# Kernel tuning notes

Hardware: AMD Instinct MI355X
Metric: run time of the kernel (lower is better)

## Reference

```python
import jax, jax.numpy as jnp
import numpy as np

B, S, D = 8, 4096, 1280   # batch, tokens, model width (== down_dim == out_dim)
R = 64                    # lora rank (mid_dim)
EMBED_W = D + R * R + D   # [down | mid | up] slices of the per-sample embed


def setup_inputs() -> dict:
    key = jax.random.key(0)
    ks = jax.random.split(key, 6)
    x = jax.random.normal(ks[0], (B, S, D), dtype=jnp.float32)
    embed = jax.random.normal(ks[1], (B, EMBED_W), dtype=jnp.float32) * 0.05
    w_down = jax.random.normal(ks[2], (R, D), dtype=jnp.float32) * 0.02
    b_down = jnp.zeros((R,), dtype=jnp.float32)
    w_up = jax.random.normal(ks[3], (D, R), dtype=jnp.float32) * 0.02
    b_up = jnp.zeros((D,), dtype=jnp.float32)
    return {"x": x, "embed": embed, "w_down": w_down, "b_down": b_down,
            "w_up": w_up, "b_up": b_up}


def reference(x, embed, w_down, b_down, w_up, b_up):
    # down_forward: modulate input channels by per-sample down weight, then lora_down
    down_w = embed[:, :D]                          # [B, D]
    h = x * down_w[:, None, :]                     # [B, S, D]
    h = jnp.einsum('bsd,rd->bsr', h, w_down) + b_down   # lora_down Linear(D->R)
    # mid_forward: per-sample [R,R] weight, x_chunk @ W.T  (batched, no python loop)
    mid_w = embed[:, D:D + R * R].reshape(B, R, R)       # [B, R, R]
    h = jnp.einsum('bsr,bqr->bsq', h, mid_w)             # [B, S, R]
    # up_forward: lora_up then modulate output channels by per-sample up weight
    out = jnp.einsum('bsr,dr->bsd', h, w_up) + b_up      # lora_up Linear(R->D)
    up_w = embed[:, -D:]                                 # [B, D]
    out = out * up_w[:, None, :]
    return out
```

## Files before the change

kernel.cpp:

```cpp
#include <hip/hip_runtime.h>
#include <hip/hip_bf16.h>

#define NB 8
#define NS 4096
#define ND 1280
#define NR 64
#define EW 6656

typedef __attribute__((ext_vector_type(4))) float f4;
typedef __attribute__((ext_vector_type(8))) short bf8;

union BF8U { bf8 v; unsigned u[4]; };

__device__ __forceinline__ unsigned short f2bf(float f) {
  union { float f; unsigned u; } v; v.f = f;
  unsigned u = v.u + 0x7FFFu + ((v.u >> 16) & 1u);
  return (unsigned short)(u >> 16);
}

__device__ __forceinline__ unsigned pk2(float a, float b) {
  __hip_bfloat162 t = __float22bfloat162_rn(float2{a, b});
  return *reinterpret_cast<unsigned*>(&t);
}

__global__ __launch_bounds__(256) void prep_all(const float* __restrict__ embed,
                                                const float* __restrict__ w_down,
                                                const float* __restrict__ w_up,
                                                const float* __restrict__ b_down,
                                                unsigned short* __restrict__ W2F,
                                                unsigned short* __restrict__ W3FB,
                                                float* __restrict__ h2bias) {
  const int blk = blockIdx.x;
  const int t   = threadIdx.x;
  if (blk < 160) {
    const int b  = blk / 20;
    const int qg = (blk % 20) / 5;
    const int dg = blk % 5;
    __shared__ float mids[16][64];
    #pragma unroll
    for (int i = 0; i < 4; ++i) {
      int idx = t + i * 256;
      mids[idx >> 6][idx & 63] = embed[b * EW + ND + qg * 1024 + idx];
    }
    __syncthreads();
    const int d = dg * 256 + t;
    float acc[16];
    #pragma unroll
    for (int q = 0; q < 16; ++q) acc[q] = 0.f;
    for (int r = 0; r < 64; r += 8) {
      float wd[8];
      #pragma unroll
      for (int u = 0; u < 8; ++u) wd[u] = w_down[(r + u) * ND + d];
      #pragma unroll
      for (int u = 0; u < 8; ++u)
        #pragma unroll
        for (int q = 0; q < 16; ++q) acc[q] += mids[q][r + u] * wd[u];
    }
    const float dwn = embed[b * EW + d];
    const int kt = d >> 5, lanehi = (d & 31) >> 3, jj = d & 7;
    #pragma unroll
    for (int q = 0; q < 16; ++q)
      W2F[(((b * 40 + kt) * 4 + qg) << 9) + (lanehi * 16 + q) * 8 + jj] = f2bf(acc[q] * dwn);
  } else if (blk < 2720) {
    const int local = blk - 160;
    const int b  = local / 320;
    const int g  = (local % 320) * 256 + t;
    const int d  = g >> 6, q = g & 63;
    const int kt = q >> 5, nt = d >> 4;
    const int lanei = ((q & 31) >> 3) * 16 + (d & 15), jj = q & 7;
    const float upw = embed[b * EW + 5376 + d];
    W3FB[(size_t)b * 81920 + ((kt * 80 + nt) * 64 + lanei) * 8 + jj] = f2bf(w_up[g] * upw);
  } else {
    #pragma unroll
    for (int ii = 0; ii < 2; ++ii) {
      int id = ii * 256 + t;
      int bb = id >> 6, q = id & 63;
      float s = 0.f;
      for (int r = 0; r < 64; ++r) s += b_down[r] * embed[bb * EW + ND + q * 64 + r];
      h2bias[id] = s;
    }
  }
}

__global__ __launch_bounds__(256, 4) void k1_h2(const float* __restrict__ x,
                                                const unsigned short* __restrict__ W2F,
                                                const float* __restrict__ h2bias,
                                                uint4* __restrict__ h2F) {
  const int tid  = threadIdx.x;
  const int lane = tid & 63;
  const int w    = tid >> 6;
  const int kh   = w >> 1;
  const int rt   = w & 1;
  const int b    = blockIdx.x & 7;
  const int tile = blockIdx.x >> 3;
  const int lo16 = lane & 15;
  const int hi4  = lane >> 4;
  const int wrow = tile * 32 + rt * 16;

  __shared__ __align__(16) char smem[32768];
  float (*xs)[2][1024]    = (float (*)[2][1024])smem;
  float (*h2p)[2][16][68] = (float (*)[2][16][68])smem;

  const float* xbase = x + ((size_t)b * NS + wrow) * ND + kh * 640;
  const unsigned short* w2b = W2F + (size_t)b * 81920;

  #define ISSUE_DMA(ck, buf)                                                         \
    _Pragma("unroll")                                                                \
    for (int it = 0; it < 4; ++it) {                                                 \
      const int rloc = it * 4 + hi4;                                                 \
      const int cf   = lo16 ^ rloc;                                                  \
      const float* src = xbase + (size_t)rloc * ND + (ck) * 64 + cf * 4;             \
      __builtin_amdgcn_global_load_lds((__attribute__((address_space(1))) void*)src, \
          (__attribute__((address_space(3))) void*)&xs[w][buf][it * 256], 16, 0, 0); \
    }

  f4 acc[4] = {};
  bf8 bw[8];

  ISSUE_DMA(0, 0)
  {
    const unsigned short* wp = w2b + (((kh * 10) * 8) << 9) + lane * 8;
    #pragma unroll
    for (int i = 0; i < 8; ++i) bw[i] = *(const bf8*)(wp + (i << 9));
  }

  for (int ck = 0; ck < 10; ++ck) {
    const int buf = ck & 1;
    bf8 bn[8];
    if (ck < 9) {
      ISSUE_DMA(ck + 1, buf ^ 1)
      const unsigned short* wp = w2b + (size_t)(((kh * 10 + ck + 1) * 8) << 9) + lane * 8;
      #pragma unroll
      for (int i = 0; i < 8; ++i) bn[i] = *(const bf8*)(wp + (i << 9));
      asm volatile("s_waitcnt vmcnt(12)" ::: "memory");
    } else {
      asm volatile("s_waitcnt vmcnt(0)" ::: "memory");
    }
    const f4* xp = (const f4*)&xs[w][buf][0];
    f4 a0 = xp[lo16 * 16 + ((hi4 * 2)     ^ lo16)];
    f4 a1 = xp[lo16 * 16 + ((hi4 * 2 + 1) ^ lo16)];
    f4 a2 = xp[lo16 * 16 + ((hi4 * 2 + 8) ^ lo16)];
    f4 a3 = xp[lo16 * 16 + ((hi4 * 2 + 9) ^ lo16)];
    BF8U af0, af1;
    af0.u[0] = pk2(a0[0], a0[1]); af0.u[1] = pk2(a0[2], a0[3]);
    af0.u[2] = pk2(a1[0], a1[1]); af0.u[3] = pk2(a1[2], a1[3]);
    af1.u[0] = pk2(a2[0], a2[1]); af1.u[1] = pk2(a2[2], a2[3]);
    af1.u[2] = pk2(a3[0], a3[1]); af1.u[3] = pk2(a3[2], a3[3]);
    #pragma unroll
    for (int nt = 0; nt < 4; ++nt)
      acc[nt] = __builtin_amdgcn_mfma_f32_16x16x32_bf16(af0.v, bw[nt], acc[nt], 0, 0, 0);
    #pragma unroll
    for (int nt = 0; nt < 4; ++nt)
      acc[nt] = __builtin_amdgcn_mfma_f32_16x16x32_bf16(af1.v, bw[4 + nt], acc[nt], 0, 0, 0);
    if (ck < 9) {
      #pragma unroll
      for (int i = 0; i < 8; ++i) bw[i] = bn[i];
    }
  }

  __syncthreads();

  #pragma unroll
  for (int nt = 0; nt < 4; ++nt)
    #pragma unroll
    for (int j = 0; j < 4; ++j)
      h2p[kh][rt][hi4 * 4 + j][nt * 16 + lo16] = acc[nt][j];
  __syncthreads();

  const int q0 = kh * 32 + hi4 * 8;
  f4 u0 = *(const f4*)&h2p[0][rt][lo16][q0];
  f4 u1 = *(const f4*)&h2p[0][rt][lo16][q0 + 4];
  f4 v0 = *(const f4*)&h2p[1][rt][lo16][q0];
  f4 v1 = *(const f4*)&h2p[1][rt][lo16][q0 + 4];
  f4 c0 = *(const f4*)(h2bias + b * 64 + q0);
  f4 c1 = *(const f4*)(h2bias + b * 64 + q0 + 4);
  float s[8];
  #pragma unroll
  for (int j = 0; j < 4; ++j) {
    s[j]     = u0[j] + v0[j] + c0[j];
    s[4 + j] = u1[j] + v1[j] + c1[j];
  }
  uint4 pk;
  pk.x = pk2(s[0], s[1]); pk.y = pk2(s[2], s[3]);
  pk.z = pk2(s[4], s[5]); pk.w = pk2(s[6], s[7]);
  h2F[(size_t)(((b * 256 + tile * 2 + rt) * 2 + kh) * 64 + lane)] = pk;
}

__global__ __launch_bounds__(256, 4) void k2_out(const uint4* __restrict__ h2F,
                                                 const float* __restrict__ embed,
                                                 const float* __restrict__ b_up,
                                                 const unsigned short* __restrict__ W3FB,
                                                 float* __restrict__ out) {
  const int tid  = threadIdx.x;
  const int lane = tid & 63;
  const int w    = tid >> 6;
  const int kh   = w >> 1;
  const int rt   = w & 1;
  const int b    = blockIdx.x & 7;
  const int t2   = blockIdx.x >> 3;
  const int lo16 = lane & 15;
  const int hi4  = lane >> 4;

  __shared__ __align__(16) float lds[4][16][36];
  __shared__ __align__(16) float pbs[1280];

  const int tile16 = t2 * 2 + rt;
  uint4 hv0 = h2F[(size_t)(((b * 256 + tile16) * 2 + 0) * 64 + lane)];
  uint4 hv1 = h2F[(size_t)(((b * 256 + tile16) * 2 + 1) * 64 + lane)];

  const float* upw = embed + b * EW + 5376;
  #pragma unroll
  for (int i = 0; i < 5; ++i) {
    const int idx = i * 256 + tid;
    pbs[idx] = b_up[idx] * upw[idx];
  }
  __syncthreads();

  BF8U ha0, ha1;
  ha0.u[0] = hv0.x; ha0.u[1] = hv0.y; ha0.u[2] = hv0.z; ha0.u[3] = hv0.w;
  ha1.u[0] = hv1.x; ha1.u[1] = hv1.y; ha1.u[2] = hv1.z; ha1.u[3] = hv1.w;

  const unsigned short* w3b = W3FB + (size_t)b * 81920;
  float* outp = out + ((size_t)b * NS + t2 * 32 + rt * 16) * ND + kh * 640;
  const int dtbase = kh * 40;

  bf8 wb00 = *(const bf8*)(w3b + (size_t)((dtbase)      * 64 + lane) * 8);
  bf8 wb01 = *(const bf8*)(w3b + (size_t)((80 + dtbase) * 64 + lane) * 8);
  bf8 wb10 = *(const bf8*)(w3b + (size_t)((dtbase + 1)      * 64 + lane) * 8);
  bf8 wb11 = *(const bf8*)(w3b + (size_t)((80 + dtbase + 1) * 64 + lane) * 8);

  for (int c = 0; c < 20; ++c) {
    f4 o0 = {}, o1 = {};
    o0 = __builtin_amdgcn_mfma_f32_16x16x32_bf16(wb00, ha0.v, o0, 0, 0, 0);
    o0 = __builtin_amdgcn_mfma_f32_16x16x32_bf16(wb01, ha1.v, o0, 0, 0, 0);
    o1 = __builtin_amdgcn_mfma_f32_16x16x32_bf16(wb10, ha0.v, o1, 0, 0, 0);
    o1 = __builtin_amdgcn_mfma_f32_16x16x32_bf16(wb11, ha1.v, o1, 0, 0, 0);
    if (c < 19) {
      const int dt = dtbase + (c + 1) * 2;
      wb00 = *(const bf8*)(w3b + (size_t)(dt * 64 + lane) * 8);
      wb01 = *(const bf8*)(w3b + (size_t)((80 + dt) * 64 + lane) * 8);
      wb10 = *(const bf8*)(w3b + (size_t)((dt + 1) * 64 + lane) * 8);
      wb11 = *(const bf8*)(w3b + (size_t)((80 + dt + 1) * 64 + lane) * 8);
    }
    #pragma unroll
    for (int i = 0; i < 2; ++i) {
      const f4 oi = i ? o1 : o0;
      const int dl = kh * 640 + c * 32 + i * 16 + hi4 * 4;
      f4 pbv = *(const f4*)&pbs[dl];
      f4 r;
      #pragma unroll
      for (int j = 0; j < 4; ++j) r[j] = oi[j] + pbv[j];
      *(f4*)&lds[w][lo16][i * 16 + hi4 * 4] = r;
    }
    #pragma unroll
    for (int k = 0; k < 2; ++k) {
      const int rr = k * 8 + (lane >> 3);
      f4 v = *(const f4*)&lds[w][rr][(lane & 7) * 4];
      *(f4*)(outp + (size_t)rr * ND + c * 32 + (lane & 7) * 4) = v;
    }
  }
}

extern "C" void kernel_launch(void* const* d_in, const int* in_sizes, int n_in,
                              void* d_out, int out_size, void* d_ws, size_t ws_size,
                              hipStream_t stream) {
  const float* x      = (const float*)d_in[0];
  const float* embed  = (const float*)d_in[1];
  const float* w_down = (const float*)d_in[2];
  const float* b_down = (const float*)d_in[3];
  const float* w_up   = (const float*)d_in[4];
  const float* b_up   = (const float*)d_in[5];
  float* out = (float*)d_out;

  char* ws = (char*)d_ws;
  unsigned short* W2F  = (unsigned short*)ws;
  unsigned short* W3FB = (unsigned short*)(ws + 1310720);
  float* h2bias        = (float*)(ws + 2621440);
  uint4* h2F           = (uint4*)(ws + 2623488);

  prep_all<<<2721, 256, 0, stream>>>(embed, w_down, w_up, b_down, W2F, W3FB, h2bias);
  k1_h2   <<<1024, 256, 0, stream>>>(x, W2F, h2bias, h2F);
  k2_out  <<<1024, 256, 0, stream>>>(h2F, embed, b_up, W3FB, out);
}
```

Before: 102.9 us.

## Fuse down-projection and up-projection kernels into one mega kernel via LDS

Merges the k1_h2 and k2_out kernels into a single kernel. The bf16 rank-64 intermediate now passes through shared memory instead of a global buffer, which removes one launch and the global write and read of h2. The per-sample up bias and h2 bias are staged in LDS at kernel start. The W3 prefetch in the output loop is also moved ahead of the MFMAs into separate registers. In exchange, register and LDS pressure per block rise and the two phases lose independent scheduling.

```diff
diff --git a/kernel.cpp b/kernel.cpp
--- a/kernel.cpp
+++ b/kernel.cpp
@@ -82,10 +82,13 @@
   }
 }
 
-__global__ __launch_bounds__(256, 4) void k1_h2(const float* __restrict__ x,
-                                                const unsigned short* __restrict__ W2F,
-                                                const float* __restrict__ h2bias,
-                                                uint4* __restrict__ h2F) {
+__global__ __launch_bounds__(256, 4) void mega(const float* __restrict__ x,
+                                               const float* __restrict__ embed,
+                                               const float* __restrict__ b_up,
+                                               const unsigned short* __restrict__ W2F,
+                                               const unsigned short* __restrict__ W3FB,
+                                               const float* __restrict__ h2bias,
+                                               float* __restrict__ out) {
   const int tid  = threadIdx.x;
   const int lane = tid & 63;
   const int w    = tid >> 6;
@@ -97,9 +100,23 @@
   const int hi4  = lane >> 4;
   const int wrow = tile * 32 + rt * 16;
 
-  __shared__ __align__(16) char smem[32768];
-  float (*xs)[2][1024]    = (float (*)[2][1024])smem;
-  float (*h2p)[2][16][68] = (float (*)[2][16][68])smem;
+  __shared__ __align__(16) char pool[32768];
+  __shared__ __align__(16) float pbs[1280];
+  __shared__ float hb[64];
+  float (*xs)[2][1024]    = (float (*)[2][1024])pool;
+  float (*h2p)[2][16][68] = (float (*)[2][16][68])pool;
+  float (*ldsT)[16][36]   = (float (*)[16][36])pool;
+  uint4* pkx              = (uint4*)(pool + 28672);
+
+  if (tid < 64) hb[tid] = h2bias[b * 64 + tid];
+  {
+    const float* upw = embed + b * EW + 5376;
+    #pragma unroll
+    for (int i = 0; i < 5; ++i) {
+      const int idx = i * 256 + tid;
+      pbs[idx] = b_up[idx] * upw[idx];
+    }
+  }
 
   const float* xbase = x + ((size_t)b * NS + wrow) * ND + kh * 640;
   const unsigned short* w2b = W2F + (size_t)b * 81920;
@@ -167,81 +184,56 @@
       h2p[kh][rt][hi4 * 4 + j][nt * 16 + lo16] = acc[nt][j];
   __syncthreads();
 
-  const int q0 = kh * 32 + hi4 * 8;
-  f4 u0 = *(const f4*)&h2p[0][rt][lo16][q0];
-  f4 u1 = *(const f4*)&h2p[0][rt][lo16][q0 + 4];
-  f4 v0 = *(const f4*)&h2p[1][rt][lo16][q0];
-  f4 v1 = *(const f4*)&h2p[1][rt][lo16][q0 + 4];
-  f4 c0 = *(const f4*)(h2bias + b * 64 + q0);
-  f4 c1 = *(const f4*)(h2bias + b * 64 + q0 + 4);
-  float s[8];
-  #pragma unroll
-  for (int j = 0; j < 4; ++j) {
-    s[j]     = u0[j] + v0[j] + c0[j];
-    s[4 + j] = u1[j] + v1[j] + c1[j];
-  }
-  uint4 pk;
-  pk.x = pk2(s[0], s[1]); pk.y = pk2(s[2], s[3]);
-  pk.z = pk2(s[4], s[5]); pk.w = pk2(s[6], s[7]);
-  h2F[(size_t)(((b * 256 + tile * 2 + rt) * 2 + kh) * 64 + lane)] = pk;
-}
-
-__global__ __launch_bounds__(256, 4) void k2_out(const uint4* __restrict__ h2F,
-                                                 const float* __restrict__ embed,
-                                                 const float* __restrict__ b_up,
-                                                 const unsigned short* __restrict__ W3FB,
-                                                 float* __restrict__ out) {
-  const int tid  = threadIdx.x;
-  const int lane = tid & 63;
-  const int w    = tid >> 6;
-  const int kh   = w >> 1;
-  const int rt   = w & 1;
-  const int b    = blockIdx.x & 7;
-  const int t2   = blockIdx.x >> 3;
-  const int lo16 = lane & 15;
-  const int hi4  = lane >> 4;
-
-  __shared__ __align__(16) float lds[4][16][36];
-  __shared__ __align__(16) float pbs[1280];
-
-  const int tile16 = t2 * 2 + rt;
-  uint4 hv0 = h2F[(size_t)(((b * 256 + tile16) * 2 + 0) * 64 + lane)];
-  uint4 hv1 = h2F[(size_t)(((b * 256 + tile16) * 2 + 1) * 64 + lane)];
-
-  const float* upw = embed + b * EW + 5376;
-  #pragma unroll
-  for (int i = 0; i < 5; ++i) {
-    const int idx = i * 256 + tid;
-    pbs[idx] = b_up[idx] * upw[idx];
+  {
+    const int q0 = kh * 32 + hi4 * 8;
+    f4 u0 = *(const f4*)&h2p[0][rt][lo16][q0];
+    f4 u1 = *(const f4*)&h2p[0][rt][lo16][q0 + 4];
+    f4 v0 = *(const f4*)&h2p[1][rt][lo16][q0];
+    f4 v1 = *(const f4*)&h2p[1][rt][lo16][q0 + 4];
+    float s[8];
+    #pragma unroll
+    for (int j = 0; j < 4; ++j) {
+      s[j]     = u0[j] + v0[j] + hb[q0 + j];
+      s[4 + j] = u1[j] + v1[j] + hb[q0 + 4 + j];
+    }
+    uint4 pk;
+    pk.x = pk2(s[0], s[1]); pk.y = pk2(s[2], s[3]);
+    pk.z = pk2(s[4], s[5]); pk.w = pk2(s[6], s[7]);
+    pkx[(rt * 2 + kh) * 64 + lane] = pk;
   }
   __syncthreads();
 
   BF8U ha0, ha1;
-  ha0.u[0] = hv0.x; ha0.u[1] = hv0.y; ha0.u[2] = hv0.z; ha0.u[3] = hv0.w;
-  ha1.u[0] = hv1.x; ha1.u[1] = hv1.y; ha1.u[2] = hv1.z; ha1.u[3] = hv1.w;
+  {
+    uint4 hv0 = pkx[(rt * 2 + 0) * 64 + lane];
+    uint4 hv1 = pkx[(rt * 2 + 1) * 64 + lane];
+    ha0.u[0] = hv0.x; ha0.u[1] = hv0.y; ha0.u[2] = hv0.z; ha0.u[3] = hv0.w;
+    ha1.u[0] = hv1.x; ha1.u[1] = hv1.y; ha1.u[2] = hv1.z; ha1.u[3] = hv1.w;
+  }
 
   const unsigned short* w3b = W3FB + (size_t)b * 81920;
-  float* outp = out + ((size_t)b * NS + t2 * 32 + rt * 16) * ND + kh * 640;
+  float* outp = out + ((size_t)b * NS + tile * 32 + rt * 16) * ND + kh * 640;
   const int dtbase = kh * 40;
 
-  bf8 wb00 = *(const bf8*)(w3b + (size_t)((dtbase)      * 64 + lane) * 8);
-  bf8 wb01 = *(const bf8*)(w3b + (size_t)((80 + dtbase) * 64 + lane) * 8);
+  bf8 wb00 = *(const bf8*)(w3b + (size_t)((dtbase)          * 64 + lane) * 8);
+  bf8 wb01 = *(const bf8*)(w3b + (size_t)((80 + dtbase)     * 64 + lane) * 8);
   bf8 wb10 = *(const bf8*)(w3b + (size_t)((dtbase + 1)      * 64 + lane) * 8);
   bf8 wb11 = *(const bf8*)(w3b + (size_t)((80 + dtbase + 1) * 64 + lane) * 8);
 
   for (int c = 0; c < 20; ++c) {
+    bf8 wn00, wn01, wn10, wn11;
+    if (c < 19) {
+      const int dt = dtbase + (c + 1) * 2;
+      wn00 = *(const bf8*)(w3b + (size_t)(dt * 64 + lane) * 8);
+      wn01 = *(const bf8*)(w3b + (size_t)((80 + dt) * 64 + lane) * 8);
+      wn10 = *(const bf8*)(w3b + (size_t)((dt + 1) * 64 + lane) * 8);
+      wn11 = *(const bf8*)(w3b + (size_t)((80 + dt + 1) * 64 + lane) * 8);
+    }
     f4 o0 = {}, o1 = {};
     o0 = __builtin_amdgcn_mfma_f32_16x16x32_bf16(wb00, ha0.v, o0, 0, 0, 0);
     o0 = __builtin_amdgcn_mfma_f32_16x16x32_bf16(wb01, ha1.v, o0, 0, 0, 0);
     o1 = __builtin_amdgcn_mfma_f32_16x16x32_bf16(wb10, ha0.v, o1, 0, 0, 0);
     o1 = __builtin_amdgcn_mfma_f32_16x16x32_bf16(wb11, ha1.v, o1, 0, 0, 0);
-    if (c < 19) {
-      const int dt = dtbase + (c + 1) * 2;
-      wb00 = *(const bf8*)(w3b + (size_t)(dt * 64 + lane) * 8);
-      wb01 = *(const bf8*)(w3b + (size_t)((80 + dt) * 64 + lane) * 8);
-      wb10 = *(const bf8*)(w3b + (size_t)((dt + 1) * 64 + lane) * 8);
-      wb11 = *(const bf8*)(w3b + (size_t)((80 + dt + 1) * 64 + lane) * 8);
-    }
     #pragma unroll
     for (int i = 0; i < 2; ++i) {
       const f4 oi = i ? o1 : o0;
@@ -250,14 +242,15 @@
       f4 r;
       #pragma unroll
       for (int j = 0; j < 4; ++j) r[j] = oi[j] + pbv[j];
-      *(f4*)&lds[w][lo16][i * 16 + hi4 * 4] = r;
+      *(f4*)&ldsT[w][lo16][i * 16 + hi4 * 4] = r;
     }
     #pragma unroll
     for (int k = 0; k < 2; ++k) {
       const int rr = k * 8 + (lane >> 3);
-      f4 v = *(const f4*)&lds[w][rr][(lane & 7) * 4];
+      f4 v = *(const f4*)&ldsT[w][rr][(lane & 7) * 4];
       *(f4*)(outp + (size_t)rr * ND + c * 32 + (lane & 7) * 4) = v;
     }
+    wb00 = wn00; wb01 = wn01; wb10 = wn10; wb11 = wn11;
   }
 }
 
@@ -276,9 +269,7 @@
   unsigned short* W2F  = (unsigned short*)ws;
   unsigned short* W3FB = (unsigned short*)(ws + 1310720);
   float* h2bias        = (float*)(ws + 2621440);
-  uint4* h2F           = (uint4*)(ws + 2623488);
 
   prep_all<<<2721, 256, 0, stream>>>(embed, w_down, w_up, b_down, W2F, W3FB, h2bias);
-  k1_h2   <<<1024, 256, 0, stream>>>(x, W2F, h2bias, h2F);
-  k2_out  <<<1024, 256, 0, stream>>>(h2F, embed, b_up, W3FB, out);
-}
+  mega    <<<1024, 256, 0, stream>>>(x, embed, b_up, W2F, W3FB, h2bias, out);
+}
```

New measurement: 113.1 us. 1.1x slower.
